# Optimization experiments

Hardware: AMD Instinct MI355X
Metric: run time of the kernel (lower is better)

Reference implementation:

```python
import jax, jax.numpy as jnp
import numpy as np

N_BASIS = 5  # identity, transpose, diag-embed(diag), row-sum broadcast, total-sum broadcast


def eq2to2_ops(x):
    """x: [B, d, n, n] -> [B, 5, d, n, n] equivariant basis ops (sums normalized by n, n^2)."""
    n = x.shape[-1]
    eye = jnp.eye(n, dtype=x.dtype)
    xt = jnp.swapaxes(x, -1, -2)
    diag = jnp.diagonal(x, axis1=-2, axis2=-1)            # [B, d, n]
    diag_emb = diag[..., :, None] * eye                   # [B, d, n, n]
    row = jnp.broadcast_to(x.sum(-1, keepdims=True) / n, x.shape)
    tot = jnp.broadcast_to(x.sum((-2, -1), keepdims=True) / (n * n), x.shape)
    return jnp.stack([x, xt, diag_emb, row, tot], axis=1)


def eq_layer(x, W, b):
    """x: [B, d_in, n, n]; W: [d_in, d_out, 5]; b: [d_out] -> [B, d_out, n, n]."""
    ops = eq2to2_ops(x)                                   # [B, 5, d_in, n, n]
    return jnp.einsum('bqdij,dsq->bsij', ops, W) + b[None, :, None, None]


def setup_inputs() -> dict:
    key = jax.random.key(0)
    ks = jax.random.split(key, 8)
    B, n, nin, nhid, ndechid, nout = 8, 256, 16, 32, 128, 1
    s = lambda fan: 1.0 / np.sqrt(fan)
    return {
        'x': jax.random.normal(ks[0], (B, n, nin), jnp.float32),
        'W1': jax.random.normal(ks[1], (2 * nin, nhid, N_BASIS), jnp.float32) * s(2 * nin * N_BASIS),
        'b1': jnp.zeros((nhid,), jnp.float32),
        'W2': jax.random.normal(ks[2], (nhid, nhid, N_BASIS), jnp.float32) * s(nhid * N_BASIS),
        'b2': jnp.zeros((nhid,), jnp.float32),
        'D1': jax.random.normal(ks[3], (nhid, ndechid), jnp.float32) * s(nhid),
        'db1': jnp.zeros((ndechid,), jnp.float32),
        'D2': jax.random.normal(ks[4], (ndechid, ndechid), jnp.float32) * s(ndechid),
        'db2': jnp.zeros((ndechid,), jnp.float32),
        'D3': jax.random.normal(ks[5], (ndechid, nout), jnp.float32) * s(ndechid),
        'db3': jnp.zeros((nout,), jnp.float32),
    }


def reference(x, W1, b1, W2, b2, D1, db1, D2, db2, D3, db3):
    B, n, d = x.shape
    eye = jnp.eye(n, dtype=x.dtype)
    # diag_embed(x.permute(0,2,1)) -> [B, d, n, n]
    x1 = jnp.swapaxes(x, 1, 2)[..., :, None] * eye
    # outer-product pairwise interactions -> [B, d, n, n]
    x2 = jnp.einsum('bid,bjd->bdij', x, x)
    h = jnp.concatenate([x1, x2], axis=1)                 # [B, 2d, n, n]
    h = jax.nn.relu(eq_layer(h, W1, b1))
    h = jax.nn.relu(eq_layer(h, W2, b2))
    h = jax.nn.relu(h.sum((-2, -1)))                      # [B, nhid]
    h = jax.nn.relu(h @ D1 + db1)
    h = jax.nn.relu(h @ D2 + db2)
    return h @ D3 + db3
```

## Files before the change

### kernel.cpp

```cpp
#include <hip/hip_runtime.h>
#include <hip/hip_bf16.h>


#define NB 8
#define NN 256
#define ND 16
#define NC 32
#define W1S 160
#define W2S 160
#define XP 20
#define NBLK 136

using bf16x8 = __attribute__((ext_vector_type(8))) __bf16;
using f32x4  = __attribute__((ext_vector_type(4))) float;

#define MFMA(a, b, c) __builtin_amdgcn_mfma_f32_16x16x32_bf16((a), (b), (c), 0, 0, 0)

#define WAVE_LDS_SYNC() do {                      \
    __builtin_amdgcn_wave_barrier();              \
    __builtin_amdgcn_s_waitcnt(0xc07f);  \
    __builtin_amdgcn_wave_barrier();              \
} while (0)

__device__ __forceinline__ bf16x8 make_av(const float* xi, const float* xj, int quad)
{
    bf16x8 av;
    if (quad < 2) {
        const float4* a = (const float4*)(xi + quad * 8);
        const float4* b = (const float4*)(xj + quad * 8);
        float4 a0 = a[0], a1 = a[1], b0 = b[0], b1 = b[1];
        av[0] = (__bf16)(a0.x * b0.x); av[1] = (__bf16)(a0.y * b0.y);
        av[2] = (__bf16)(a0.z * b0.z); av[3] = (__bf16)(a0.w * b0.w);
        av[4] = (__bf16)(a1.x * b1.x); av[5] = (__bf16)(a1.y * b1.y);
        av[6] = (__bf16)(a1.z * b1.z); av[7] = (__bf16)(a1.w * b1.w);
    } else {
        #pragma unroll
        for (int j = 0; j < 8; ++j) av[j] = (__bf16)0.f;
    }
    return av;
}

__device__ __forceinline__ unsigned pack2(float lo, float hi)
{
    union { __bf16 b[2]; unsigned u; } p;
    p.b[0] = (__bf16)lo; p.b[1] = (__bf16)hi;
    return p.u;
}

__global__ __launch_bounds__(256) void kC_rows(
    const float* __restrict__ x, const float* __restrict__ W1,
    const float* __restrict__ b1, const float* __restrict__ W2,
    float* __restrict__ T1g, float* __restrict__ R1, float* __restrict__ Dg1,
    float* __restrict__ TotP, float* __restrict__ CD2, float* __restrict__ CR2,
    __bf16* __restrict__ BQt, __bf16* __restrict__ Wpm,
    float* __restrict__ Wt4)
{
    const int TI = blockIdx.x, b = blockIdx.y, t = threadIdx.x;
    __shared__ __align__(16) float  sX[NN][XP];
    __shared__ __align__(16) float  sW1[2 * ND][W1S];
    __shared__ __align__(16) __bf16 sBQ[NC][48];
    __shared__ float part[16][ND + 1];
    __shared__ float sS[ND];
    __shared__ float sRT[4][NC], sDgL[4][NC], sRow[4][NC], sDiag[4][NC];

    {
        const float4* xg4 = (const float4*)(x + b * NN * ND);
        #pragma unroll
        for (int kk = 0; kk < 4; ++kk) {
            int idx = t + kk * 256;
            int row = idx >> 2, c4 = idx & 3;
            *(float4*)&sX[row][c4 * 4] = xg4[idx];
        }
    }
    {
        const float4* wg1 = (const float4*)W1;
        float4* sw1 = (float4*)&sW1[0][0];
        #pragma unroll
        for (int kk = 0; kk < 5; ++kk) sw1[t + kk * 256] = wg1[t + kk * 256];
    }
    #pragma unroll
    for (int kk = 0; kk < 2; ++kk) {
        int idx = t + kk * 256; int c = idx >> 4, k = idx & 15;
        sBQ[c][k] = (__bf16)(W1[(ND + k) * W1S + c * 5 + 0]
                           + W1[(ND + k) * W1S + c * 5 + 1]);
    }
    #pragma unroll
    for (int kk = 0; kk < 4; ++kk) {
        int idx = t + kk * 256;
        sBQ[idx >> 5][16 + (idx & 31)] = (__bf16)0.f;
    }
    __syncthreads();

    {
        int rr = t >> 4, d = t & 15;
        float p = 0.f;
        #pragma unroll
        for (int k = 0; k < 16; ++k) p += sX[rr + (k << 4)][d];
        part[rr][d] = p;
    }
    if (TI == 0 && b == 0) {
        if (t < 192) ((float4*)BQt)[t] = ((const float4*)&sBQ[0][0])[t];
        for (int idx = t; idx < 1024; idx += 256) {
            int s = idx >> 5, kp = idx & 31;
            int c = ((kp & 1) << 4) | (kp >> 1);
            float w0 = W2[c * W2S + s * 5 + 0], w1 = W2[c * W2S + s * 5 + 1];
            Wpm[s * 40 + kp]        = (__bf16)((w0 + w1) * 0.5f);
            Wpm[1280 + s * 40 + kp] = (__bf16)((w0 - w1) * 0.5f);
        }
        for (int idx = t; idx < 1024; idx += 256)
            Wt4[(idx >> 5) * 32 + (idx & 31)] = W2[(idx >> 5) * W2S + (idx & 31) * 5 + 4];
    }
    __syncthreads();
    if (t < ND) {
        float s = 0.f;
        #pragma unroll
        for (int k = 0; k < 16; ++k) s += part[k][t];
        sS[t] = s;
    }
    __syncthreads();
    if (t < 128) {
        int i_l = t >> 5, c = t & 31;
        int gi = TI * 4 + i_l;
        float r = 0.f, dg = 0.f, tt = 0.f;
        #pragma unroll
        for (int d = 0; d < ND; ++d) {
            float xi = sX[gi][d], sd = sS[d];
            const float* wa = &sW1[d][c * 5];
            const float* wb = &sW1[ND + d][c * 5];
            r  += xi * wa[3] + xi * sd * wb[3];
            dg += xi * (wa[0] + wa[1] + wa[2]) + xi * xi * wb[2];
            tt += sd * wa[4] + sd * sd * wb[4];
        }
        r *= (1.f / 256.f);
        float t1 = tt * (1.f / 65536.f) + b1[c];
        R1[(b * NN + gi) * NC + c] = r;
        Dg1[(b * NN + gi) * NC + c] = dg;
        sRT[i_l][c] = t1 + r;
        sDgL[i_l][c] = dg;
        if (TI == 0 && i_l == 0) T1g[b * NC + c] = t1;
    }
    __syncthreads();

    const int ln = t & 63, wv = t >> 6;
    const int m = ln & 15, quad = ln >> 4;
    const int gi = TI * 4 + wv;
    bf16x8 bq0 = *(const bf16x8*)&sBQ[m][8 * quad];
    bf16x8 bq1 = *(const bf16x8*)&sBQ[m + 16][8 * quad];
    float rt0 = sRT[wv][m], rt1 = sRT[wv][m + 16];
    float dg0 = sDgL[wv][m], dg1 = sDgL[wv][m + 16];
    f32x4 zero = {0.f, 0.f, 0.f, 0.f};
    float rs0 = 0.f, rs1 = 0.f;

    for (int jg = 0; jg < 8; ++jg) {
        #pragma unroll
        for (int gg = 0; gg < 2; ++gg) {
            int jrow = jg * 32 + gg * 16 + m;
            bf16x8 av = make_av(&sX[gi][0], &sX[jrow][0], quad);
            f32x4 q0 = MFMA(av, bq0, zero);
            f32x4 q1 = MFMA(av, bq1, zero);
            int jb = jg * 32 + gg * 16 + quad * 4;
            #pragma unroll
            for (int r = 0; r < 4; ++r) {
                float v0 = q0[r] + rt0, v1 = q1[r] + rt1;
                bool dgf = (jb + r == gi);
                if (dgf) { v0 += dg0; v1 += dg1; }
                float h0 = fmaxf(v0, 0.f), h1 = fmaxf(v1, 0.f);
                if (dgf) { sDiag[wv][m] = h0; sDiag[wv][m + 16] = h1; }
                rs0 += h0; rs1 += h1;
            }
        }
    }
    rs0 += __shfl_down(rs0, 32, 64); rs0 += __shfl_down(rs0, 16, 64);
    rs1 += __shfl_down(rs1, 32, 64); rs1 += __shfl_down(rs1, 16, 64);
    if (ln < 16) { sRow[wv][ln] = rs0; sRow[wv][ln + 16] = rs1; }
    __syncthreads();
    if (t < NC)
        TotP[TI * (NB * NC) + b * NC + t]
            = sRow[0][t] + sRow[1][t] + sRow[2][t] + sRow[3][t];
    if (t < 128) {
        int i_l = t >> 5, s = t & 31;
        int gi2 = TI * 4 + i_l;
        float cd = 0.f, cr = 0.f;
        #pragma unroll
        for (int c = 0; c < NC; ++c) {
            cd += sDiag[i_l][c] * W2[c * W2S + s * 5 + 2];
            cr += sRow[i_l][c]  * W2[c * W2S + s * 5 + 3];
        }
        CD2[(b * NN + gi2) * NC + s] = cd;
        CR2[(b * NN + gi2) * NC + s] = cr * (1.f / 256.f);
    }
}

__global__ __launch_bounds__(256) void kD_main(
    const float* __restrict__ x,
    const __bf16* __restrict__ BQt, const __bf16* __restrict__ Wpm,
    const float* __restrict__ Wt4, const float* __restrict__ b2,
    const float* __restrict__ T1g, const float* __restrict__ R1g,
    const float* __restrict__ Dg1g, const float* __restrict__ CD2g,
    const float* __restrict__ CR2g, const float* __restrict__ TotP,
    float* __restrict__ GP)
{
    const int b = blockIdx.y, t = threadIdx.x;
    int TI = 0, rem = blockIdx.x;
    while (rem >= 16 - TI) { rem -= 16 - TI; ++TI; }
    const int TJ = TI + rem;
    const bool diagblk = (TI == TJ), mirror = !diagblk;

    __shared__ __align__(16) __bf16 sUw[4][16][40];
    __shared__ __align__(16) __bf16 sVw[4][16][40];
    __shared__ __align__(16) __bf16 sBQ[NC][48];
    __shared__ __align__(16) __bf16 sWp[NC][40], sWm[NC][40];
    __shared__ __align__(16) float sXI[16][XP], sXJ[16][XP];
    __shared__ float sTot[NC], sCT2[NC];
    __shared__ float red[4][NC];

    if (t < 128) {
        const float4* xg4 = (const float4*)(x + b * NN * ND);
        int half = t >> 6, idx = t & 63;
        int row = idx >> 2, c4 = idx & 3;
        int base = (half ? TJ : TI) * 16;
        float4 v = xg4[(base + row) * 4 + c4];
        float* dst = half ? &sXJ[row][c4 * 4] : &sXI[row][c4 * 4];
        *(float4*)dst = v;
    }
    if (t < 192) ((float4*)&sBQ[0][0])[t] = ((const float4*)BQt)[t];
    {
        const float4* wsrc = (const float4*)Wpm;
        #pragma unroll
        for (int i = t; i < 320; i += 256) {
            float4 v = wsrc[i];
            if (i < 160) ((float4*)&sWp[0][0])[i] = v;
            else         ((float4*)&sWm[0][0])[i - 160] = v;
        }
    }
    if (t < NC) {
        float tot = 0.f;
        #pragma unroll
        for (int k = 0; k < 64; ++k) tot += TotP[k * (NB * NC) + b * NC + t];
        sTot[t] = tot;
    }
    if (t < 64) {
        WAVE_LDS_SYNC();
        if (t < NC) {
            float ct = 0.f;
            #pragma unroll
            for (int c = 0; c < NC; ++c) ct += sTot[c] * Wt4[c * 32 + t];
            sCT2[t] = ct * (1.f / 65536.f) + b2[t];
        }
    }

    const int ln = t & 63, wv = t >> 6;
    const int m = ln & 15, quad = ln >> 4;

    const float* R1b = R1g + b * NN * NC;
    const float* Dgb = Dg1g + b * NN * NC;
    const float* CDb = CD2g + b * NN * NC;
    const float* CRb = CR2g + b * NN * NC;
    float t10 = T1g[b * NC + m], t11 = T1g[b * NC + m + 16];
    float rti[4][2], dgi[4][2], rtj[4][2];
    float cri[4][2], cdi[4][2], crj[4][2];
    #pragma unroll
    for (int gg = 0; gg < 4; ++gg) {
        int rowI = TI * 16 + wv * 4 + gg;
        rti[gg][0] = R1b[rowI * NC + m] + t10;
        rti[gg][1] = R1b[rowI * NC + m + 16] + t11;
        dgi[gg][0] = Dgb[rowI * NC + m];
        dgi[gg][1] = Dgb[rowI * NC + m + 16];
        cri[gg][0] = CRb[rowI * NC + m];
        cri[gg][1] = CRb[rowI * NC + m + 16];
        cdi[gg][0] = CDb[rowI * NC + m];
        cdi[gg][1] = CDb[rowI * NC + m + 16];
    }
    #pragma unroll
    for (int r = 0; r < 4; ++r) {
        int rowJ = TJ * 16 + quad * 4 + r;
        rtj[r][0] = R1b[rowJ * NC + m] + t10;
        rtj[r][1] = R1b[rowJ * NC + m + 16] + t11;
        crj[r][0] = CRb[rowJ * NC + m];
        crj[r][1] = CRb[rowJ * NC + m + 16];
    }
    __syncthreads();

    float ct0 = sCT2[m], ct1 = sCT2[m + 16];
    #pragma unroll
    for (int gg = 0; gg < 4; ++gg) { cri[gg][0] += ct0; cri[gg][1] += ct1; }
    #pragma unroll
    for (int r = 0; r < 4; ++r) { crj[r][0] += ct0; crj[r][1] += ct1; }

    bf16x8 bq0 = *(const bf16x8*)&sBQ[m][8 * quad];
    bf16x8 bq1 = *(const bf16x8*)&sBQ[m + 16][8 * quad];
    bf16x8 wp0 = *(const bf16x8*)&sWp[m][8 * quad];
    bf16x8 wp1 = *(const bf16x8*)&sWp[m + 16][8 * quad];
    bf16x8 wm0 = *(const bf16x8*)&sWm[m][8 * quad];
    bf16x8 wm1 = *(const bf16x8*)&sWm[m + 16][8 * quad];
    __bf16* Uw = &sUw[wv][0][0];
    __bf16* Vw = &sVw[wv][0][0];
    f32x4 zero = {0.f, 0.f, 0.f, 0.f};
    float acc0 = 0.f, acc1 = 0.f;

    #pragma unroll
    for (int gg = 0; gg < 4; ++gg) {
        int g = wv * 4 + gg;
        __builtin_amdgcn_wave_barrier();
        {
            bf16x8 av = make_av(&sXI[g][0], &sXJ[m][0], quad);
            f32x4 q0 = MFMA(av, bq0, zero);
            f32x4 q1 = MFMA(av, bq1, zero);
            #pragma unroll
            for (int r = 0; r < 4; ++r) {
                int tj = quad * 4 + r;
                float a0 = q0[r] + rti[gg][0], b0 = q0[r] + rtj[r][0];
                float a1 = q1[r] + rti[gg][1], b1 = q1[r] + rtj[r][1];
                if (diagblk && tj == g) {
                    a0 += dgi[gg][0]; b0 = a0;
                    a1 += dgi[gg][1]; b1 = a1;
                }
                float hA0 = fmaxf(a0, 0.f), hB0 = fmaxf(b0, 0.f);
                float hA1 = fmaxf(a1, 0.f), hB1 = fmaxf(b1, 0.f);
                *(unsigned*)&Uw[tj * 40 + 2 * m] = pack2(hA0 + hB0, hA1 + hB1);
                *(unsigned*)&Vw[tj * 40 + 2 * m] = pack2(hA0 - hB0, hA1 - hB1);
            }
        }
        WAVE_LDS_SYNC();
        {
            bf16x8 ua = *(const bf16x8*)&Uw[m * 40 + 8 * quad];
            bf16x8 va = *(const bf16x8*)&Vw[m * 40 + 8 * quad];
            f32x4 P0 = MFMA(ua, wp0, zero);
            f32x4 M0 = MFMA(va, wm0, zero);
            f32x4 P1 = MFMA(ua, wp1, zero);
            f32x4 M1 = MFMA(va, wm1, zero);
            #pragma unroll
            for (int r = 0; r < 4; ++r) {
                int tj = quad * 4 + r;
                float a1v = P0[r] + M0[r] + cri[gg][0];
                float a2v = P0[r] - M0[r] + crj[r][0];
                float e1 = P1[r] + M1[r] + cri[gg][1];
                float e2 = P1[r] - M1[r] + crj[r][1];
                if (diagblk && tj == g) { a1v += cdi[gg][0]; e1 += cdi[gg][1]; }
                acc0 += fmaxf(a1v, 0.f); acc1 += fmaxf(e1, 0.f);
                if (mirror) { acc0 += fmaxf(a2v, 0.f); acc1 += fmaxf(e2, 0.f); }
            }
        }
    }

    acc0 += __shfl_down(acc0, 32, 64); acc0 += __shfl_down(acc0, 16, 64);
    acc1 += __shfl_down(acc1, 32, 64); acc1 += __shfl_down(acc1, 16, 64);
    if (ln < 16) { red[wv][ln] = acc0; red[wv][ln + 16] = acc1; }
    __syncthreads();
    if (t < NC)
        GP[blockIdx.x * (NB * NC) + b * NC + t]
            = red[0][t] + red[1][t] + red[2][t] + red[3][t];
}

__global__ __launch_bounds__(256) void k5_mlp(
    const float* __restrict__ GP, const float* __restrict__ D1,
    const float* __restrict__ db1, const float* __restrict__ D2,
    const float* __restrict__ db2, const float* __restrict__ D3,
    const float* __restrict__ db3, float* __restrict__ out)
{
    int b = blockIdx.x, t = threadIdx.x;
    __shared__ float sGp[8][NC], a[NC], h2s[128], r2[2];
    {
        int q = t >> 5, s = t & 31;
        float p = 0.f;
        for (int k = q; k < NBLK; k += 8) p += GP[k * (NB * NC) + b * NC + s];
        sGp[q][s] = p;
    }
    __syncthreads();
    if (t < NC) {
        float s = 0.f;
        #pragma unroll
        for (int q = 0; q < 8; ++q) s += sGp[q][t];
        a[t] = fmaxf(s, 0.f);
    }
    __syncthreads();
    if (t < 128) {
        float acc = db1[t];
        #pragma unroll
        for (int s = 0; s < NC; ++s) acc += a[s] * D1[s * 128 + t];
        h2s[t] = fmaxf(acc, 0.f);
    }
    __syncthreads();
    if (t < 128) {
        float acc2 = db2[t];
        #pragma unroll 8
        for (int u = 0; u < 128; ++u) acc2 += h2s[u] * D2[u * 128 + t];
        float h3 = fmaxf(acc2, 0.f);
        float v = h3 * D3[t];
        #pragma unroll
        for (int off = 32; off > 0; off >>= 1) v += __shfl_down(v, off, 64);
        if ((t & 63) == 0) r2[t >> 6] = v;
    }
    __syncthreads();
    if (t == 0) out[b] = r2[0] + r2[1] + db3[0];
}

extern "C" void kernel_launch(void* const* d_in, const int* in_sizes, int n_in,
                              void* d_out, int out_size, void* d_ws, size_t ws_size,
                              hipStream_t stream)
{
    const float* x   = (const float*)d_in[0];
    const float* W1  = (const float*)d_in[1];
    const float* b1  = (const float*)d_in[2];
    const float* W2  = (const float*)d_in[3];
    const float* b2  = (const float*)d_in[4];
    const float* D1  = (const float*)d_in[5];
    const float* db1 = (const float*)d_in[6];
    const float* D2  = (const float*)d_in[7];
    const float* db2 = (const float*)d_in[8];
    const float* D3  = (const float*)d_in[9];
    const float* db3 = (const float*)d_in[10];
    float* out = (float*)d_out;

    float* w = (float*)d_ws;
    float* pT1   = w; w += NB * NC;
    float* pTotP = w; w += 64 * NB * NC;
    float* pGP   = w; w += NBLK * NB * NC;
    float* pR1   = w; w += NB * NN * NC;
    float* pDg1  = w; w += NB * NN * NC;
    float* pCD2  = w; w += NB * NN * NC;
    float* pCR2  = w; w += NB * NN * NC;
    __bf16* pBQt = (__bf16*)w; w += 768;
    __bf16* pWpm = (__bf16*)w; w += 1280;
    float* pWt4  = w; w += 1024;

    hipLaunchKernelGGL(kC_rows, dim3(64, NB), dim3(256), 0, stream,
                       x, W1, b1, W2, pT1, pR1, pDg1, pTotP, pCD2, pCR2,
                       pBQt, pWpm, pWt4);
    hipLaunchKernelGGL(kD_main, dim3(NBLK, NB), dim3(256), 0, stream,
                       x, pBQt, pWpm, pWt4, b2, pT1, pR1, pDg1, pCD2, pCR2,
                       pTotP, pGP);
    hipLaunchKernelGGL(k5_mlp, dim3(NB), dim3(256), 0, stream,
                       pGP, D1, db1, D2, db2, D3, db3, out);
}
```

Before: 110.0 us.

## Coarsen row and pair-tile work per block in both main kernels

kC_rows now handles 8 rows per block instead of 4, giving each wave two rows and halving the grid to 32 blocks per batch. kD_main now handles a 2x2 super-tile of 16x16 tiles per block, which cuts the grid from 136 to 36 blocks per batch and skips the redundant lower pair inside diagonal super-tiles. The aim is to amortise the per-block setup (weight staging, TotP reduction, row vector loads) and shorten the partial-sum reductions. In exchange there are fewer blocks to fill the GPU and more registers per thread, which may reduce occupancy and parallelism.

```diff
diff --git a/kernel.cpp b/kernel.cpp
--- a/kernel.cpp
+++ b/kernel.cpp
@@ -9,7 +9,8 @@
 #define W1S 160
 #define W2S 160
 #define XP 20
-#define NBLK 136
+#define KC_NT 32
+#define NSP 36
 
 using bf16x8 = __attribute__((ext_vector_type(8))) __bf16;
 using f32x4  = __attribute__((ext_vector_type(4))) float;
@@ -61,7 +62,7 @@
     __shared__ __align__(16) __bf16 sBQ[NC][48];
     __shared__ float part[16][ND + 1];
     __shared__ float sS[ND];
-    __shared__ float sRT[4][NC], sDgL[4][NC], sRow[4][NC], sDiag[4][NC];
+    __shared__ float sRT[8][NC], sDgL[8][NC], sRow[8][NC], sDiag[8][NC];
 
     {
         const float4* xg4 = (const float4*)(x + b * NN * ND);
@@ -118,9 +119,9 @@
         sS[t] = s;
     }
     __syncthreads();
-    if (t < 128) {
-        int i_l = t >> 5, c = t & 31;
-        int gi = TI * 4 + i_l;
+    {
+        int lr = t >> 5, c = t & 31;
+        int gi = TI * 8 + lr;
         float r = 0.f, dg = 0.f, tt = 0.f;
         #pragma unroll
         for (int d = 0; d < ND; ++d) {
@@ -135,56 +136,74 @@
         float t1 = tt * (1.f / 65536.f) + b1[c];
         R1[(b * NN + gi) * NC + c] = r;
         Dg1[(b * NN + gi) * NC + c] = dg;
-        sRT[i_l][c] = t1 + r;
-        sDgL[i_l][c] = dg;
-        if (TI == 0 && i_l == 0) T1g[b * NC + c] = t1;
+        sRT[lr][c] = t1 + r;
+        sDgL[lr][c] = dg;
+        if (TI == 0 && lr == 0) T1g[b * NC + c] = t1;
     }
     __syncthreads();
 
     const int ln = t & 63, wv = t >> 6;
     const int m = ln & 15, quad = ln >> 4;
-    const int gi = TI * 4 + wv;
+    const int lr0 = wv * 2, lr1 = lr0 + 1;
+    const int gi0 = TI * 8 + lr0, gi1 = gi0 + 1;
     bf16x8 bq0 = *(const bf16x8*)&sBQ[m][8 * quad];
     bf16x8 bq1 = *(const bf16x8*)&sBQ[m + 16][8 * quad];
-    float rt0 = sRT[wv][m], rt1 = sRT[wv][m + 16];
-    float dg0 = sDgL[wv][m], dg1 = sDgL[wv][m + 16];
+    float rt00 = sRT[lr0][m], rt01 = sRT[lr0][m + 16];
+    float rt10 = sRT[lr1][m], rt11 = sRT[lr1][m + 16];
+    float dg00 = sDgL[lr0][m], dg01 = sDgL[lr0][m + 16];
+    float dg10 = sDgL[lr1][m], dg11 = sDgL[lr1][m + 16];
     f32x4 zero = {0.f, 0.f, 0.f, 0.f};
-    float rs0 = 0.f, rs1 = 0.f;
+    float rsA0 = 0.f, rsA1 = 0.f, rsB0 = 0.f, rsB1 = 0.f;
 
     for (int jg = 0; jg < 8; ++jg) {
         #pragma unroll
         for (int gg = 0; gg < 2; ++gg) {
             int jrow = jg * 32 + gg * 16 + m;
-            bf16x8 av = make_av(&sX[gi][0], &sX[jrow][0], quad);
-            f32x4 q0 = MFMA(av, bq0, zero);
-            f32x4 q1 = MFMA(av, bq1, zero);
+            bf16x8 av0 = make_av(&sX[gi0][0], &sX[jrow][0], quad);
+            bf16x8 av1 = make_av(&sX[gi1][0], &sX[jrow][0], quad);
+            f32x4 q00 = MFMA(av0, bq0, zero);
+            f32x4 q01 = MFMA(av0, bq1, zero);
+            f32x4 q10 = MFMA(av1, bq0, zero);
+            f32x4 q11 = MFMA(av1, bq1, zero);
             int jb = jg * 32 + gg * 16 + quad * 4;
             #pragma unroll
             for (int r = 0; r < 4; ++r) {
-                float v0 = q0[r] + rt0, v1 = q1[r] + rt1;
-                bool dgf = (jb + r == gi);
-                if (dgf) { v0 += dg0; v1 += dg1; }
-                float h0 = fmaxf(v0, 0.f), h1 = fmaxf(v1, 0.f);
-                if (dgf) { sDiag[wv][m] = h0; sDiag[wv][m + 16] = h1; }
-                rs0 += h0; rs1 += h1;
+                float v00 = q00[r] + rt00, v01 = q01[r] + rt01;
+                float v10 = q10[r] + rt10, v11 = q11[r] + rt11;
+                bool d0 = (jb + r == gi0), d1 = (jb + r == gi1);
+                if (d0) { v00 += dg00; v01 += dg01; }
+                if (d1) { v10 += dg10; v11 += dg11; }
+                float h00 = fmaxf(v00, 0.f), h01 = fmaxf(v01, 0.f);
+                float h10 = fmaxf(v10, 0.f), h11 = fmaxf(v11, 0.f);
+                if (d0) { sDiag[lr0][m] = h00; sDiag[lr0][m + 16] = h01; }
+                if (d1) { sDiag[lr1][m] = h10; sDiag[lr1][m + 16] = h11; }
+                rsA0 += h00; rsA1 += h01; rsB0 += h10; rsB1 += h11;
             }
         }
     }
-    rs0 += __shfl_down(rs0, 32, 64); rs0 += __shfl_down(rs0, 16, 64);
-    rs1 += __shfl_down(rs1, 32, 64); rs1 += __shfl_down(rs1, 16, 64);
-    if (ln < 16) { sRow[wv][ln] = rs0; sRow[wv][ln + 16] = rs1; }
-    __syncthreads();
-    if (t < NC)
-        TotP[TI * (NB * NC) + b * NC + t]
-            = sRow[0][t] + sRow[1][t] + sRow[2][t] + sRow[3][t];
-    if (t < 128) {
-        int i_l = t >> 5, s = t & 31;
-        int gi2 = TI * 4 + i_l;
+    rsA0 += __shfl_down(rsA0, 32, 64); rsA0 += __shfl_down(rsA0, 16, 64);
+    rsA1 += __shfl_down(rsA1, 32, 64); rsA1 += __shfl_down(rsA1, 16, 64);
+    rsB0 += __shfl_down(rsB0, 32, 64); rsB0 += __shfl_down(rsB0, 16, 64);
+    rsB1 += __shfl_down(rsB1, 32, 64); rsB1 += __shfl_down(rsB1, 16, 64);
+    if (ln < 16) {
+        sRow[lr0][ln] = rsA0; sRow[lr0][ln + 16] = rsA1;
+        sRow[lr1][ln] = rsB0; sRow[lr1][ln + 16] = rsB1;
+    }
+    __syncthreads();
+    if (t < NC) {
+        float s = 0.f;
+        #pragma unroll
+        for (int k = 0; k < 8; ++k) s += sRow[k][t];
+        TotP[TI * (NB * NC) + b * NC + t] = s;
+    }
+    {
+        int lr = t >> 5, s = t & 31;
+        int gi2 = TI * 8 + lr;
         float cd = 0.f, cr = 0.f;
         #pragma unroll
         for (int c = 0; c < NC; ++c) {
-            cd += sDiag[i_l][c] * W2[c * W2S + s * 5 + 2];
-            cr += sRow[i_l][c]  * W2[c * W2S + s * 5 + 3];
+            cd += sDiag[lr][c] * W2[c * W2S + s * 5 + 2];
+            cr += sRow[lr][c]  * W2[c * W2S + s * 5 + 3];
         }
         CD2[(b * NN + gi2) * NC + s] = cd;
         CR2[(b * NN + gi2) * NC + s] = cr * (1.f / 256.f);
@@ -201,27 +220,25 @@
     float* __restrict__ GP)
 {
     const int b = blockIdx.y, t = threadIdx.x;
-    int TI = 0, rem = blockIdx.x;
-    while (rem >= 16 - TI) { rem -= 16 - TI; ++TI; }
-    const int TJ = TI + rem;
-    const bool diagblk = (TI == TJ), mirror = !diagblk;
+    int SI = 0, rem = blockIdx.x;
+    while (rem >= 8 - SI) { rem -= 8 - SI; ++SI; }
+    const int SJ = SI + rem;
+    const bool diagSP = (SI == SJ);
 
     __shared__ __align__(16) __bf16 sUw[4][16][40];
     __shared__ __align__(16) __bf16 sVw[4][16][40];
     __shared__ __align__(16) __bf16 sBQ[NC][48];
     __shared__ __align__(16) __bf16 sWp[NC][40], sWm[NC][40];
-    __shared__ __align__(16) float sXI[16][XP], sXJ[16][XP];
+    __shared__ __align__(16) float sXt[4][16][XP];
     __shared__ float sTot[NC], sCT2[NC];
     __shared__ float red[4][NC];
 
-    if (t < 128) {
+    {
         const float4* xg4 = (const float4*)(x + b * NN * ND);
-        int half = t >> 6, idx = t & 63;
+        int tile = t >> 6, idx = t & 63;
         int row = idx >> 2, c4 = idx & 3;
-        int base = (half ? TJ : TI) * 16;
-        float4 v = xg4[(base + row) * 4 + c4];
-        float* dst = half ? &sXJ[row][c4 * 4] : &sXI[row][c4 * 4];
-        *(float4*)dst = v;
+        int gt = (tile < 2) ? (2 * SI + tile) : (2 * SJ + (tile - 2));
+        *(float4*)&sXt[tile][row][c4 * 4] = xg4[(gt * 16 + row) * 4 + c4];
     }
     if (t < 192) ((float4*)&sBQ[0][0])[t] = ((const float4*)BQt)[t];
     {
@@ -236,7 +253,7 @@
     if (t < NC) {
         float tot = 0.f;
         #pragma unroll
-        for (int k = 0; k < 64; ++k) tot += TotP[k * (NB * NC) + b * NC + t];
+        for (int k = 0; k < KC_NT; ++k) tot += TotP[k * (NB * NC) + b * NC + t];
         sTot[t] = tot;
     }
     if (t < 64) {
@@ -257,35 +274,43 @@
     const float* CDb = CD2g + b * NN * NC;
     const float* CRb = CR2g + b * NN * NC;
     float t10 = T1g[b * NC + m], t11 = T1g[b * NC + m + 16];
-    float rti[4][2], dgi[4][2], rtj[4][2];
-    float cri[4][2], cdi[4][2], crj[4][2];
-    #pragma unroll
-    for (int gg = 0; gg < 4; ++gg) {
-        int rowI = TI * 16 + wv * 4 + gg;
-        rti[gg][0] = R1b[rowI * NC + m] + t10;
-        rti[gg][1] = R1b[rowI * NC + m + 16] + t11;
-        dgi[gg][0] = Dgb[rowI * NC + m];
-        dgi[gg][1] = Dgb[rowI * NC + m + 16];
-        cri[gg][0] = CRb[rowI * NC + m];
-        cri[gg][1] = CRb[rowI * NC + m + 16];
-        cdi[gg][0] = CDb[rowI * NC + m];
-        cdi[gg][1] = CDb[rowI * NC + m + 16];
-    }
-    #pragma unroll
-    for (int r = 0; r < 4; ++r) {
-        int rowJ = TJ * 16 + quad * 4 + r;
-        rtj[r][0] = R1b[rowJ * NC + m] + t10;
-        rtj[r][1] = R1b[rowJ * NC + m + 16] + t11;
-        crj[r][0] = CRb[rowJ * NC + m];
-        crj[r][1] = CRb[rowJ * NC + m + 16];
-    }
+    float rti[2][4][2], dgi[2][4][2], cri[2][4][2], cdi[2][4][2];
+    float rtj[2][4][2], crj[2][4][2];
+    #pragma unroll
+    for (int a = 0; a < 2; ++a)
+        #pragma unroll
+        for (int gg = 0; gg < 4; ++gg) {
+            int rowI = (2 * SI + a) * 16 + wv * 4 + gg;
+            rti[a][gg][0] = R1b[rowI * NC + m] + t10;
+            rti[a][gg][1] = R1b[rowI * NC + m + 16] + t11;
+            dgi[a][gg][0] = Dgb[rowI * NC + m];
+            dgi[a][gg][1] = Dgb[rowI * NC + m + 16];
+            cri[a][gg][0] = CRb[rowI * NC + m];
+            cri[a][gg][1] = CRb[rowI * NC + m + 16];
+            cdi[a][gg][0] = CDb[rowI * NC + m];
+            cdi[a][gg][1] = CDb[rowI * NC + m + 16];
+        }
+    #pragma unroll
+    for (int bb = 0; bb < 2; ++bb)
+        #pragma unroll
+        for (int r = 0; r < 4; ++r) {
+            int rowJ = (2 * SJ + bb) * 16 + quad * 4 + r;
+            rtj[bb][r][0] = R1b[rowJ * NC + m] + t10;
+            rtj[bb][r][1] = R1b[rowJ * NC + m + 16] + t11;
+            crj[bb][r][0] = CRb[rowJ * NC + m];
+            crj[bb][r][1] = CRb[rowJ * NC + m + 16];
+        }
     __syncthreads();
 
     float ct0 = sCT2[m], ct1 = sCT2[m + 16];
     #pragma unroll
-    for (int gg = 0; gg < 4; ++gg) { cri[gg][0] += ct0; cri[gg][1] += ct1; }
-    #pragma unroll
-    for (int r = 0; r < 4; ++r) { crj[r][0] += ct0; crj[r][1] += ct1; }
+    for (int a = 0; a < 2; ++a)
+        #pragma unroll
+        for (int gg = 0; gg < 4; ++gg) { cri[a][gg][0] += ct0; cri[a][gg][1] += ct1; }
+    #pragma unroll
+    for (int bb = 0; bb < 2; ++bb)
+        #pragma unroll
+        for (int r = 0; r < 4; ++r) { crj[bb][r][0] += ct0; crj[bb][r][1] += ct1; }
 
     bf16x8 bq0 = *(const bf16x8*)&sBQ[m][8 * quad];
     bf16x8 bq1 = *(const bf16x8*)&sBQ[m + 16][8 * quad];
@@ -299,46 +324,56 @@
     float acc0 = 0.f, acc1 = 0.f;
 
     #pragma unroll
-    for (int gg = 0; gg < 4; ++gg) {
-        int g = wv * 4 + gg;
-        __builtin_amdgcn_wave_barrier();
-        {
-            bf16x8 av = make_av(&sXI[g][0], &sXJ[m][0], quad);
-            f32x4 q0 = MFMA(av, bq0, zero);
-            f32x4 q1 = MFMA(av, bq1, zero);
-            #pragma unroll
-            for (int r = 0; r < 4; ++r) {
-                int tj = quad * 4 + r;
-                float a0 = q0[r] + rti[gg][0], b0 = q0[r] + rtj[r][0];
-                float a1 = q1[r] + rti[gg][1], b1 = q1[r] + rtj[r][1];
-                if (diagblk && tj == g) {
-                    a0 += dgi[gg][0]; b0 = a0;
-                    a1 += dgi[gg][1]; b1 = a1;
+    for (int pr = 0; pr < 4; ++pr) {
+        const int a = pr >> 1, bb = pr & 1;
+        if (diagSP && a == 1 && bb == 0) continue;
+        const bool diagblk = diagSP && (a == bb);
+        const bool mirror = !diagblk;
+        const float* XI = &sXt[a][0][0];
+        const float* XJ = &sXt[2 + bb][0][0];
+
+        #pragma unroll
+        for (int gg = 0; gg < 4; ++gg) {
+            int g = wv * 4 + gg;
+            __builtin_amdgcn_wave_barrier();
+            {
+                bf16x8 av = make_av(XI + g * XP, XJ + m * XP, quad);
+                f32x4 q0 = MFMA(av, bq0, zero);
+                f32x4 q1 = MFMA(av, bq1, zero);
+                #pragma unroll
+                for (int r = 0; r < 4; ++r) {
+                    int tj = quad * 4 + r;
+                    float a0 = q0[r] + rti[a][gg][0], b0 = q0[r] + rtj[bb][r][0];
+                    float a1 = q1[r] + rti[a][gg][1], b1 = q1[r] + rtj[bb][r][1];
+                    if (diagblk && tj == g) {
+                        a0 += dgi[a][gg][0]; b0 = a0;
+                        a1 += dgi[a][gg][1]; b1 = a1;
+                    }
+                    float hA0 = fmaxf(a0, 0.f), hB0 = fmaxf(b0, 0.f);
+                    float hA1 = fmaxf(a1, 0.f), hB1 = fmaxf(b1, 0.f);
+                    *(unsigned*)&Uw[tj * 40 + 2 * m] = pack2(hA0 + hB0, hA1 + hB1);
+                    *(unsigned*)&Vw[tj * 40 + 2 * m] = pack2(hA0 - hB0, hA1 - hB1);
                 }
-                float hA0 = fmaxf(a0, 0.f), hB0 = fmaxf(b0, 0.f);
-                float hA1 = fmaxf(a1, 0.f), hB1 = fmaxf(b1, 0.f);
-                *(unsigned*)&Uw[tj * 40 + 2 * m] = pack2(hA0 + hB0, hA1 + hB1);
-                *(unsigned*)&Vw[tj * 40 + 2 * m] = pack2(hA0 - hB0, hA1 - hB1);
             }
-        }
-        WAVE_LDS_SYNC();
-        {
-            bf16x8 ua = *(const bf16x8*)&Uw[m * 40 + 8 * quad];
-            bf16x8 va = *(const bf16x8*)&Vw[m * 40 + 8 * quad];
-            f32x4 P0 = MFMA(ua, wp0, zero);
-            f32x4 M0 = MFMA(va, wm0, zero);
-            f32x4 P1 = MFMA(ua, wp1, zero);
-            f32x4 M1 = MFMA(va, wm1, zero);
-            #pragma unroll
-            for (int r = 0; r < 4; ++r) {
-                int tj = quad * 4 + r;
-                float a1v = P0[r] + M0[r] + cri[gg][0];
-                float a2v = P0[r] - M0[r] + crj[r][0];
-                float e1 = P1[r] + M1[r] + cri[gg][1];
-                float e2 = P1[r] - M1[r] + crj[r][1];
-                if (diagblk && tj == g) { a1v += cdi[gg][0]; e1 += cdi[gg][1]; }
-                acc0 += fmaxf(a1v, 0.f); acc1 += fmaxf(e1, 0.f);
-                if (mirror) { acc0 += fmaxf(a2v, 0.f); acc1 += fmaxf(e2, 0.f); }
+            WAVE_LDS_SYNC();
+            {
+                bf16x8 ua = *(const bf16x8*)&Uw[m * 40 + 8 * quad];
+                bf16x8 va = *(const bf16x8*)&Vw[m * 40 + 8 * quad];
+                f32x4 P0 = MFMA(ua, wp0, zero);
+                f32x4 M0 = MFMA(va, wm0, zero);
+                f32x4 P1 = MFMA(ua, wp1, zero);
+                f32x4 M1 = MFMA(va, wm1, zero);
+                #pragma unroll
+                for (int r = 0; r < 4; ++r) {
+                    int tj = quad * 4 + r;
+                    float a1v = P0[r] + M0[r] + cri[a][gg][0];
+                    float a2v = P0[r] - M0[r] + crj[bb][r][0];
+                    float e1 = P1[r] + M1[r] + cri[a][gg][1];
+                    float e2 = P1[r] - M1[r] + crj[bb][r][1];
+                    if (diagblk && tj == g) { a1v += cdi[a][gg][0]; e1 += cdi[a][gg][1]; }
+                    acc0 += fmaxf(a1v, 0.f); acc1 += fmaxf(e1, 0.f);
+                    if (mirror) { acc0 += fmaxf(a2v, 0.f); acc1 += fmaxf(e2, 0.f); }
+                }
             }
         }
     }
@@ -363,7 +398,7 @@
     {
         int q = t >> 5, s = t & 31;
         float p = 0.f;
-        for (int k = q; k < NBLK; k += 8) p += GP[k * (NB * NC) + b * NC + s];
+        for (int k = q; k < NSP; k += 8) p += GP[k * (NB * NC) + b * NC + s];
         sGp[q][s] = p;
     }
     __syncthreads();
@@ -414,8 +449,8 @@
 
     float* w = (float*)d_ws;
     float* pT1   = w; w += NB * NC;
-    float* pTotP = w; w += 64 * NB * NC;
-    float* pGP   = w; w += NBLK * NB * NC;
+    float* pTotP = w; w += KC_NT * NB * NC;
+    float* pGP   = w; w += NSP * NB * NC;
     float* pR1   = w; w += NB * NN * NC;
     float* pDg1  = w; w += NB * NN * NC;
     float* pCD2  = w; w += NB * NN * NC;
@@ -424,10 +459,10 @@
     __bf16* pWpm = (__bf16*)w; w += 1280;
     float* pWt4  = w; w += 1024;
 
-    hipLaunchKernelGGL(kC_rows, dim3(64, NB), dim3(256), 0, stream,
+    hipLaunchKernelGGL(kC_rows, dim3(KC_NT, NB), dim3(256), 0, stream,
                        x, W1, b1, W2, pT1, pR1, pDg1, pTotP, pCD2, pCR2,
                        pBQt, pWpm, pWt4);
-    hipLaunchKernelGGL(kD_main, dim3(NBLK, NB), dim3(256), 0, stream,
+    hipLaunchKernelGGL(kD_main, dim3(NSP, NB), dim3(256), 0, stream,
                        x, pBQt, pWpm, pWt4, b2, pT1, pR1, pDg1, pCD2, pCR2,
                        pTotP, pGP);
     hipLaunchKernelGGL(k5_mlp, dim3(NB), dim3(256), 0, stream,
```

Measured after the change: 112.2 us. +2.0%, slower.
